# Performance work log

Measured on AMD Instinct MI355X. Metric: run time of the kernel, lower is better.

The kernel has to match this reference:

```python
import jax, jax.numpy as jnp
import numpy as np

B, S, H, E, R, K = 8, 2048, 2048, 8, 16, 3
ALPHA = 0.5
LAMBDA_COV = 0.5
BETA_ENT = 0.1
TEMP_LO, TEMP_HI = 0.5, 1.5
SCALE_T = 2.0   # lora scaling (alpha/r) teacher
SCALE_S = 2.0   # lora scaling student
EPS = 1e-8


def setup_inputs() -> dict:
    key = jax.random.key(0)
    ks = jax.random.split(key, 16)
    tg = jax.random.uniform(ks[0], (B, S, E)) + 1e-3
    tg = tg / tg.sum(-1, keepdims=True)            # teacher gate probabilities
    sg = jax.random.uniform(ks[1], (B, S, E)) + 1e-3
    sg = sg / sg.sum(-1, keepdims=True)            # student gate probabilities
    th = jax.random.normal(ks[2], (B, S, H), jnp.float32)
    sh = jax.random.normal(ks[3], (B, S, H), jnp.float32)
    mask = jnp.ones((B, S), jnp.int32)
    un = jax.random.uniform(ks[4], (K, B, S, E))   # MC sampling noise
    inv = 1.0 / np.sqrt(H)
    W_t = jax.random.normal(ks[5], (H, H), jnp.float32) * inv
    b_t = jnp.zeros((H,), jnp.float32)
    A_t = jax.random.normal(ks[6], (R, H), jnp.float32) * 0.02
    B_t = jax.random.normal(ks[7], (E, H, R), jnp.float32) * 0.02
    W_s = jax.random.normal(ks[8], (H, H), jnp.float32) * inv
    b_s = jnp.zeros((H,), jnp.float32)
    A_s = jax.random.normal(ks[9], (R, H), jnp.float32) * 0.02
    B_s = jax.random.normal(ks[10], (E, H, R), jnp.float32) * 0.02
    temperature = jnp.float32(1.0)
    return dict(teacher_gates=tg, student_gates=sg,
                teacher_hidden_states=th, student_hidden_states=sh,
                attention_mask=mask, uniform_noise=un,
                W_t=W_t, b_t=b_t, A_t=A_t, B_t=B_t,
                W_s=W_s, b_s=b_s, A_s=A_s, B_s=B_s,
                temperature=temperature)


def _mse_all_experts(th, sh, W_t, b_t, A_t, B_t, W_s, b_s, A_s, B_s):
    """MSE(student_expert_hidden, teacher_expert_hidden) for ALL experts at once.
    expert_hidden = x@W^T + b + scale * (x@A^T) @ B_e^T. Expanding the squared
    difference avoids materializing [B,S,E,H]."""
    base_t = th @ W_t.T + b_t                      # [B,S,H]
    base_s = sh @ W_s.T + b_s                      # [B,S,H]
    a_t = th @ A_t.T                               # [B,S,R]
    a_s = sh @ A_s.T                               # [B,S,R]
    d = base_s - base_t                            # [B,S,H]
    mean_base = jnp.mean(d * d, axis=-1)           # [B,S]
    # cross terms: (1/H) d . (scale * a @ B_e^T)
    proj_s = jnp.einsum('bsh,ehr->bser', d, B_s)   # [B,S,E,R]
    proj_t = jnp.einsum('bsh,ehr->bser', d, B_t)
    cross = SCALE_S * jnp.einsum('bser,bsr->bse', proj_s, a_s) \
          - SCALE_T * jnp.einsum('bser,bsr->bse', proj_t, a_t)
    # quadratic lora terms via per-expert Gram matrices [E,R,R]
    G_ss = jnp.einsum('ehr,ehq->erq', B_s, B_s)
    G_st = jnp.einsum('ehr,ehq->erq', B_s, B_t)
    G_tt = jnp.einsum('ehr,ehq->erq', B_t, B_t)
    q_ss = jnp.einsum('bsr,erq,bsq->bse', a_s, G_ss, a_s)
    q_st = jnp.einsum('bsr,erq,bsq->bse', a_s, G_st, a_t)
    q_tt = jnp.einsum('bsr,erq,bsq->bse', a_t, G_tt, a_t)
    quad = SCALE_S * SCALE_S * q_ss - 2.0 * SCALE_S * SCALE_T * q_st + SCALE_T * SCALE_T * q_tt
    return mean_base[..., None] + (2.0 / H) * cross + (1.0 / H) * quad  # [B,S,E]


def _method_a(teacher_gates, student_gates, mse_all, uniform_noise, mask_f):
    """Vectorized MC expert sampling with alpha-renormalization (lax.scan over K)."""
    gumbel = -jnp.log(-jnp.log(uniform_noise * (1.0 - 2e-7) + 1e-7))  # [K,B,S,E]

    def step(p, g):  # p: current (renormalized) probs [B,S,E]
        idx = jnp.argmax(jnp.log(p) + g, axis=-1)          # multinomial sample [B,S]
        oh = jax.nn.one_hot(idx, E, dtype=p.dtype)          # [B,S,E]
        w = jnp.sum(p * oh, -1)                             # importance weight [B,S]
        mse_k = jnp.sum(mse_all * oh, -1)                   # gathered expert MSE
        sg_k = jnp.sum(student_gates * oh, -1)              # student gate at sampled expert
        mw = mask_f * w
        feat = jnp.sum(mw * mse_k)
        wsum = jnp.sum(mw)
        t_counts = jnp.sum(mw[..., None] * oh, axis=(0, 1))           # [E]
        s_counts = jnp.sum((mask_f * sg_k)[..., None] * oh, axis=(0, 1))
        p_new = p * (1.0 + (ALPHA - 1.0) * oh)
        p_new = p_new / jnp.sum(p_new, -1, keepdims=True)
        return p_new, (feat, wsum, t_counts, s_counts)

    _, (feats, wsums, tcs, scs) = jax.lax.scan(step, teacher_gates, gumbel)
    total_feat = feats.sum()
    total_w = wsums.sum()
    t_counts = tcs.sum(0)
    s_counts = scs.sum(0)

    feat_loss = total_feat / jnp.maximum(total_w, 1e-8)
    t_avg = t_counts / t_counts.sum() + EPS
    s_avg = s_counts / s_counts.sum() + EPS
    t_avg = t_avg / t_avg.sum()
    s_avg = s_avg / s_avg.sum()
    # F.kl_div(s.log(), t, reduction='batchmean') on 1-D input divides by E
    coverage_kl = jnp.sum(t_avg * (jnp.log(t_avg) - jnp.log(s_avg))) / E
    return feat_loss, coverage_kl


def reference(teacher_gates, student_gates, teacher_hidden_states, student_hidden_states,
              attention_mask, uniform_noise, W_t, b_t, A_t, B_t, W_s, b_s, A_s, B_s,
              temperature):
    mask_f = attention_mask.astype(teacher_gates.dtype)
    mse_all = _mse_all_experts(teacher_hidden_states, student_hidden_states,
                               W_t, b_t, A_t, B_t, W_s, b_s, A_s, B_s)
    feat_loss, coverage_kl = _method_a(teacher_gates, student_gates, mse_all,
                                       uniform_noise, mask_f)
    method_a_total = feat_loss + LAMBDA_COV * coverage_kl
    # Method B: temperature-entropy router distillation
    temp_c = jnp.clip(temperature, TEMP_LO, TEMP_HI)
    s_temp = jax.nn.softmax(student_gates / temp_c, axis=-1)
    # F.kl_div(s_temp.log(), teacher, 'batchmean') divides by batch dim B
    temp_kl = jnp.sum(teacher_gates * (jnp.log(teacher_gates) - jnp.log(s_temp))) / B
    entropy = -jnp.sum(student_gates * jnp.log(student_gates), axis=-1)
    entropy_loss = -jnp.mean(entropy)
    method_b_total = temp_kl + BETA_ENT * entropy_loss
    # [feat, coverage_kl, method_a_total, temp_kl, entropy, method_b_total, temperature]
    return jnp.stack([feat_loss, coverage_kl, method_a_total,
                      temp_kl, entropy_loss, method_b_total, temp_c])
```

## Files before the change

### kernel.cpp

```cpp
#include <hip/hip_runtime.h>
#include <math.h>

typedef unsigned short u16;
typedef unsigned int u32;
typedef float f32x4 __attribute__((ext_vector_type(4)));
typedef __bf16 bf16x8 __attribute__((ext_vector_type(8)));

#define NTOK 16384
#define HD   2048
#define KX   4096

__device__ __forceinline__ u16 f2bf(float f) {
  u32 u = __float_as_uint(f);
  u32 r = (u + 0x7fffu + ((u >> 16) & 1u)) >> 16;
  return (u16)r;
}
__device__ __forceinline__ float bf2f(u16 s) { return __uint_as_float(((u32)s) << 16); }

__device__ __forceinline__ void gload_lds16(const void* g, void* l) {
  __builtin_amdgcn_global_load_lds((const __attribute__((address_space(1))) u32*)g,
                                   (__attribute__((address_space(3))) u32*)l, 16, 0, 0);
}

__global__ void zero_k(float* a, int n) {
  int i = blockIdx.x * 256 + threadIdx.x;
  if (i < n) a[i] = 0.f;
}

__global__ void make_bias_k(const float* __restrict__ b_t, const float* __restrict__ b_s,
                            float* __restrict__ db) {
  int i = blockIdx.x * 256 + threadIdx.x;
  if (i < HD) db[i] = b_s[i] - b_t[i];
}

__global__ __launch_bounds__(256) void convert_X_k(const float* __restrict__ th,
                                                   const float* __restrict__ sh,
                                                   u16* __restrict__ X) {
  size_t t = (size_t)blockIdx.x * 256 + threadIdx.x;
  int n = (int)(t >> 9);
  int k = ((int)t & 511) * 8;
  const float* src = (k < HD) ? (th + (size_t)n * HD + k) : (sh + (size_t)n * HD + (k - HD));
  float4 v0 = *(const float4*)src;
  float4 v1 = *(const float4*)(src + 4);
  uint4 pk;
  pk.x = (u32)f2bf(v0.x) | ((u32)f2bf(v0.y) << 16);
  pk.y = (u32)f2bf(v0.z) | ((u32)f2bf(v0.w) << 16);
  pk.z = (u32)f2bf(v1.x) | ((u32)f2bf(v1.y) << 16);
  pk.w = (u32)f2bf(v1.z) | ((u32)f2bf(v1.w) << 16);
  *(uint4*)(X + t * 8) = pk;
}

__global__ __launch_bounds__(256) void convert_W_k(const float* __restrict__ W_t,
                                                   const float* __restrict__ W_s,
                                                   const float* __restrict__ A_t,
                                                   const float* __restrict__ A_s,
                                                   u16* __restrict__ Wc,
                                                   u16* __restrict__ WcA) {
  size_t t = (size_t)blockIdx.x * 256 + threadIdx.x;
  int nr = (int)(t >> 9);
  int k = ((int)t & 511) * 8;
  float f[8];
#pragma unroll
  for (int j = 0; j < 8; ++j) f[j] = 0.f;
  u16* dst;
  if (nr < HD) {
    dst = Wc + (size_t)nr * KX + k;
    if (k < HD) {
      const float* s = W_t + (size_t)nr * HD + k;
#pragma unroll
      for (int j = 0; j < 8; ++j) f[j] = -s[j];
    } else {
      const float* s = W_s + (size_t)nr * HD + (k - HD);
#pragma unroll
      for (int j = 0; j < 8; ++j) f[j] = s[j];
    }
  } else {
    int nr2 = nr - HD;
    dst = WcA + (size_t)nr2 * KX + k;
    if (nr2 < 16) {
      if (k < HD) {
        const float* s = A_t + (size_t)nr2 * HD + k;
#pragma unroll
        for (int j = 0; j < 8; ++j) f[j] = s[j];
      }
    } else if (nr2 < 32) {
      if (k >= HD) {
        const float* s = A_s + (size_t)(nr2 - 16) * HD + (k - HD);
#pragma unroll
        for (int j = 0; j < 8; ++j) f[j] = s[j];
      }
    }
  }
  uint4 pk;
  pk.x = (u32)f2bf(f[0]) | ((u32)f2bf(f[1]) << 16);
  pk.y = (u32)f2bf(f[2]) | ((u32)f2bf(f[3]) << 16);
  pk.z = (u32)f2bf(f[4]) | ((u32)f2bf(f[5]) << 16);
  pk.w = (u32)f2bf(f[6]) | ((u32)f2bf(f[7]) << 16);
  *(uint4*)dst = pk;
}

__global__ __launch_bounds__(256) void convert_Bc_k(const float* __restrict__ Bs_,
                                                    const float* __restrict__ Bt_,
                                                    u16* __restrict__ Bc) {
  size_t t = (size_t)blockIdx.x * 256 + threadIdx.x;
  int c = (int)(t >> 8);
  int h = ((int)t & 255) * 8;
  const float* src = (c < 128) ? Bs_ : Bt_;
  int e = (c & 127) >> 4, r = c & 15;
  const float* base = src + (size_t)e * HD * 16 + (size_t)h * 16 + r;
  float f[8];
#pragma unroll
  for (int j = 0; j < 8; ++j) f[j] = base[(size_t)j * 16];
  uint4 pk;
  pk.x = (u32)f2bf(f[0]) | ((u32)f2bf(f[1]) << 16);
  pk.y = (u32)f2bf(f[2]) | ((u32)f2bf(f[3]) << 16);
  pk.z = (u32)f2bf(f[4]) | ((u32)f2bf(f[5]) << 16);
  pk.w = (u32)f2bf(f[6]) | ((u32)f2bf(f[7]) << 16);
  *(uint4*)(Bc + t * 8) = pk;
}

__global__ __launch_bounds__(256) void gram_k(const float* __restrict__ Bs_,
                                              const float* __restrict__ Bt_,
                                              float* __restrict__ grams) {
  __shared__ float ss[128 * 16];
  __shared__ float st[128 * 16];
  const int e = blockIdx.x >> 4;
  const int ch = blockIdx.x & 15;
  const int tid = threadIdx.x;
  const float* bs = Bs_ + (size_t)e * HD * 16 + (size_t)ch * 128 * 16;
  const float* bt = Bt_ + (size_t)e * HD * 16 + (size_t)ch * 128 * 16;
#pragma unroll
  for (int j = 0; j < 8; ++j) {
    int i = tid + j * 256;
    ss[i] = bs[i];
    st[i] = bt[i];
  }
  __syncthreads();
  const int r = tid >> 4, q = tid & 15;
  float gss = 0.f, gst = 0.f, gtt = 0.f;
  for (int hh = 0; hh < 128; ++hh) {
    float vsr = ss[hh * 16 + r], vsq = ss[hh * 16 + q];
    float vtr = st[hh * 16 + r], vtq = st[hh * 16 + q];
    gss += vsr * vsq;
    gst += vsr * vtq;
    gtt += vtr * vtq;
  }
  atomicAdd(&grams[e * 256 + r * 16 + q], gss);
  atomicAdd(&grams[2048 + e * 256 + r * 16 + q], gst);
  atomicAdd(&grams[4096 + e * 256 + r * 16 + q], gtt);
}

__global__ __launch_bounds__(512, 2) void gemm256_k(const u16* __restrict__ A,
                                                    const u16* __restrict__ Bm,
                                                    u16* __restrict__ D,
                                                    const float* __restrict__ bias) {
  __shared__ u16 As[2][16384];
  __shared__ u16 Bs[2][16384];
  const int tid = threadIdx.x;
  const int w = tid >> 6, l = tid & 63;
  const int id = blockIdx.x;
  const int tile = (id & 7) * 64 + (id >> 3);
  const int m0 = (tile & 63) * 256;
  const int n0 = (tile >> 6) * 256;
  const int wm = (w >> 2) * 128;
  const int wn = (w & 3) * 64;

  f32x4 acc[8][4] = {};

  const int rlo = w * 8 + (l >> 3);
  const int csw = ((l & 7) ^ (l >> 3)) * 8;
  const u16* gA = A + (size_t)(m0 + rlo) * KX + csw;
  const u16* gB = Bm + (size_t)(n0 + rlo) * KX + csw;

  for (int t = 0; t < 64; ++t) {
    const int b = t & 1;
    if (t == 0) {
#pragma unroll
      for (int i = 0; i < 4; ++i) {
        gload_lds16(gA + (size_t)i * 64 * KX, &As[0][i * 4096 + w * 512]);
        gload_lds16(gB + (size_t)i * 64 * KX, &Bs[0][i * 4096 + w * 512]);
      }
    }
    __syncthreads();
    if (t < 63) {
      const u16* ga = gA + (size_t)(t + 1) * 64;
      const u16* gb = gB + (size_t)(t + 1) * 64;
#pragma unroll
      for (int i = 0; i < 4; ++i) {
        gload_lds16(ga + (size_t)i * 64 * KX, &As[b ^ 1][i * 4096 + w * 512]);
        gload_lds16(gb + (size_t)i * 64 * KX, &Bs[b ^ 1][i * 4096 + w * 512]);
      }
    }
#pragma unroll
    for (int ks = 0; ks < 2; ++ks) {
      bf16x8 bfr[4], afr[4];
#pragma unroll
      for (int n = 0; n < 4; ++n) {
        int row = wn + n * 16 + (l & 15);
        int off = (row * 64 + ks * 32 + (l >> 4) * 8) ^ ((row & 7) * 8);
        bfr[n] = *(const bf16x8*)&Bs[b][off];
      }
#pragma unroll
      for (int mm = 0; mm < 4; ++mm) {
        int row = wm + mm * 16 + (l & 15);
        int off = (row * 64 + ks * 32 + (l >> 4) * 8) ^ ((row & 7) * 8);
        afr[mm] = *(const bf16x8*)&As[b][off];
      }
      __builtin_amdgcn_s_setprio(1);
#pragma unroll
      for (int mm = 0; mm < 4; ++mm)
#pragma unroll
        for (int n = 0; n < 4; ++n)
          acc[mm][n] = __builtin_amdgcn_mfma_f32_16x16x32_bf16(afr[mm], bfr[n], acc[mm][n], 0, 0, 0);
      __builtin_amdgcn_s_setprio(0);
#pragma unroll
      for (int mm = 0; mm < 4; ++mm) {
        int row = wm + 64 + mm * 16 + (l & 15);
        int off = (row * 64 + ks * 32 + (l >> 4) * 8) ^ ((row & 7) * 8);
        afr[mm] = *(const bf16x8*)&As[b][off];
      }
      __builtin_amdgcn_s_setprio(1);
#pragma unroll
      for (int mm = 0; mm < 4; ++mm)
#pragma unroll
        for (int n = 0; n < 4; ++n)
          acc[4 + mm][n] = __builtin_amdgcn_mfma_f32_16x16x32_bf16(afr[mm], bfr[n], acc[4 + mm][n], 0, 0, 0);
      __builtin_amdgcn_s_setprio(0);
    }
  }

#pragma unroll
  for (int mi = 0; mi < 8; ++mi) {
#pragma unroll
    for (int ni = 0; ni < 4; ++ni) {
      int row0 = m0 + wm + mi * 16 + (l >> 4) * 4;
      int col = n0 + wn + ni * 16 + (l & 15);
      float badd = bias[col];
      f32x4 v = acc[mi][ni];
#pragma unroll
      for (int j = 0; j < 4; ++j)
        D[(size_t)(row0 + j) * HD + col] = f2bf(v[j] + badd);
    }
  }
}

__global__ __launch_bounds__(256) void gemm_bt_k(const u16* __restrict__ A, int lda,
                                                 const u16* __restrict__ Bm, int ldb,
                                                 int K, float* __restrict__ Cp, int ldc,
                                                 int store_n) {
  __shared__ u16 Asl[128 * 32];
  __shared__ u16 Bsl[128 * 32];
  const int tid = threadIdx.x;
  const int wave = tid >> 6;
  const int lane = tid & 63;
  const int m0 = blockIdx.x * 128;
  const int n0 = blockIdx.y * 128;
  const int wm = (wave >> 1) * 64;
  const int wn = (wave & 1) * 64;
  f32x4 acc[4][4] = {};

  const int srow = wave * 32 + (lane >> 2);
  const int scol = (lane & 3) * 8;
  const u16* gA = A + (size_t)(m0 + srow) * lda + scol;
  const u16* gB = Bm + (size_t)(n0 + srow) * ldb + scol;
  u16* lA = Asl + wave * 1024;
  u16* lB = Bsl + wave * 1024;

  for (int k0 = 0; k0 < K; k0 += 32) {
    gload_lds16(gA + k0, lA);
    gload_lds16(gA + k0 + (size_t)16 * lda, lA + 512);
    gload_lds16(gB + k0, lB);
    gload_lds16(gB + k0 + (size_t)16 * ldb, lB + 512);
    __syncthreads();
    bf16x8 af[4], bff[4];
#pragma unroll
    for (int mi = 0; mi < 4; ++mi)
      af[mi] = *(const bf16x8*)&Asl[(wm + mi * 16 + (lane & 15)) * 32 + (lane >> 4) * 8];
#pragma unroll
    for (int ni = 0; ni < 4; ++ni)
      bff[ni] = *(const bf16x8*)&Bsl[(wn + ni * 16 + (lane & 15)) * 32 + (lane >> 4) * 8];
#pragma unroll
    for (int mi = 0; mi < 4; ++mi)
#pragma unroll
      for (int ni = 0; ni < 4; ++ni)
        acc[mi][ni] = __builtin_amdgcn_mfma_f32_16x16x32_bf16(af[mi], bff[ni], acc[mi][ni], 0, 0, 0);
    __syncthreads();
  }

#pragma unroll
  for (int mi = 0; mi < 4; ++mi) {
#pragma unroll
    for (int ni = 0; ni < 4; ++ni) {
      int row0 = m0 + wm + mi * 16 + (lane >> 4) * 4;
      int col = n0 + wn + ni * 16 + (lane & 15);
      if (col < store_n) {
        f32x4 v = acc[mi][ni];
#pragma unroll
        for (int j = 0; j < 4; ++j)
          Cp[(size_t)(row0 + j) * ldc + col] = v[j];
      }
    }
  }
}

__global__ __launch_bounds__(256) void token_k(const u16* __restrict__ D,
                                               const float* __restrict__ aV,
                                               const float* __restrict__ proj,
                                               const float* __restrict__ grams,
                                               const float* __restrict__ tg,
                                               const float* __restrict__ sg,
                                               const float* __restrict__ un,
                                               const int* __restrict__ maskp,
                                               const float* __restrict__ temp,
                                               float* __restrict__ accum) {
  __shared__ float blk[20];
  if (threadIdx.x < 20) blk[threadIdx.x] = 0.f;
  __syncthreads();
  const int wave = threadIdx.x >> 6, lane = threadIdx.x & 63;
  const int n = blockIdx.x * 4 + wave;
  const u16* drow = D + (size_t)n * HD;

  float ssum = 0.f;
#pragma unroll
  for (int j = 0; j < 4; ++j) {
    uint4 v = *(const uint4*)(drow + j * 512 + lane * 8);
    u32 wv;
    float f;
    wv = v.x; f = bf2f((u16)(wv & 0xffff)); ssum += f * f; f = bf2f((u16)(wv >> 16)); ssum += f * f;
    wv = v.y; f = bf2f((u16)(wv & 0xffff)); ssum += f * f; f = bf2f((u16)(wv >> 16)); ssum += f * f;
    wv = v.z; f = bf2f((u16)(wv & 0xffff)); ssum += f * f; f = bf2f((u16)(wv >> 16)); ssum += f * f;
    wv = v.w; f = bf2f((u16)(wv & 0xffff)); ssum += f * f; f = bf2f((u16)(wv >> 16)); ssum += f * f;
  }
#pragma unroll
  for (int m = 1; m < 64; m <<= 1) ssum += __shfl_xor(ssum, m);
  const float mean_base = ssum * (1.0f / (float)HD);

  const float* arow = aV + (size_t)n * 32;
  float a_tv[16], a_sv[16];
#pragma unroll
  for (int r = 0; r < 16; ++r) {
    a_tv[r] = arow[r];
    a_sv[r] = arow[16 + r];
  }

  const int e = lane & 7;
  const int pp = lane >> 3;
  const float* Ps = proj + (size_t)n * 256 + e * 16;
  const float* Pt = Ps + 128;
  const float* Gss = grams + e * 256;
  const float* Gst = grams + 2048 + e * 256;
  const float* Gtt = grams + 4096 + e * 256;
  float crossp = 0.f, qss = 0.f, qst = 0.f, qtt = 0.f;
#pragma unroll
  for (int rr = 0; rr < 2; ++rr) {
    int r = pp * 2 + rr;
    float asr = arow[16 + r];
    float atr = arow[r];
    crossp += 2.0f * Ps[r] * asr - 2.0f * Pt[r] * atr;
    const float* gssr = Gss + r * 16;
    const float* gstr = Gst + r * 16;
    const float* gttr = Gtt + r * 16;
    float vss = 0.f, vst = 0.f, vtt = 0.f;
#pragma unroll
    for (int q = 0; q < 16; ++q) {
      vss += gssr[q] * a_sv[q];
      vst += gstr[q] * a_tv[q];
      vtt += gttr[q] * a_tv[q];
    }
    qss += asr * vss;
    qst += asr * vst;
    qtt += atr * vtt;
  }
#pragma unroll
  for (int m = 8; m < 64; m <<= 1) {
    crossp += __shfl_xor(crossp, m);
    qss += __shfl_xor(qss, m);
    qst += __shfl_xor(qst, m);
    qtt += __shfl_xor(qtt, m);
  }
  float quad = 4.0f * qss - 8.0f * qst + 4.0f * qtt;
  float my_mse = mean_base + (2.0f / (float)HD) * crossp + (1.0f / (float)HD) * quad;

  float p[8], gt[8], gs[8];
#pragma unroll
  for (int i = 0; i < 8; ++i) {
    gt[i] = tg[(size_t)n * 8 + i];
    gs[i] = sg[(size_t)n * 8 + i];
    p[i] = gt[i];
  }
  const float mf = (float)maskp[n];
  float feat = 0.f, wsum = 0.f;
  float tc[8] = {0, 0, 0, 0, 0, 0, 0, 0};
  float sc[8] = {0, 0, 0, 0, 0, 0, 0, 0};
#pragma unroll
  for (int k = 0; k < 3; ++k) {
    int idx = 0;
    float best = -1e30f;
#pragma unroll
    for (int i = 0; i < 8; ++i) {
      float u = un[((size_t)k * NTOK + n) * 8 + i];
      float g = -logf(-logf(u * (1.0f - 2e-7f) + 1e-7f));
      float s = logf(p[i]) + g;
      if (s > best) { best = s; idx = i; }
    }
    float wgt = 0.f, sgi = 0.f;
#pragma unroll
    for (int i = 0; i < 8; ++i)
      if (i == idx) { wgt = p[i]; sgi = gs[i]; }
    float mse_k = __shfl(my_mse, idx);
    feat += mf * wgt * mse_k;
    wsum += mf * wgt;
#pragma unroll
    for (int i = 0; i < 8; ++i)
      if (i == idx) { tc[i] += mf * wgt; sc[i] += mf * sgi; }
    float sum = 0.f;
#pragma unroll
    for (int i = 0; i < 8; ++i) {
      if (i == idx) p[i] *= 0.5f;
      sum += p[i];
    }
#pragma unroll
    for (int i = 0; i < 8; ++i) p[i] /= sum;
  }

  float tcl = fminf(fmaxf(temp[0], 0.5f), 1.5f);
  float invt = 1.0f / tcl;
  float x[8];
  float xm = -1e30f;
#pragma unroll
  for (int i = 0; i < 8; ++i) { x[i] = gs[i] * invt; xm = fmaxf(xm, x[i]); }
  float sx = 0.f;
#pragma unroll
  for (int i = 0; i < 8; ++i) sx += expf(x[i] - xm);
  float lse = xm + logf(sx);
  float tkl = 0.f, ent = 0.f;
#pragma unroll
  for (int i = 0; i < 8; ++i) {
    tkl += gt[i] * (logf(gt[i]) - (x[i] - lse));
    ent -= gs[i] * logf(gs[i]);
  }

  if (lane == 0) {
    atomicAdd(&blk[0], feat);
    atomicAdd(&blk[1], wsum);
#pragma unroll
    for (int i = 0; i < 8; ++i) {
      atomicAdd(&blk[2 + i], tc[i]);
      atomicAdd(&blk[10 + i], sc[i]);
    }
    atomicAdd(&blk[18], tkl);
    atomicAdd(&blk[19], ent);
  }
  __syncthreads();
  if (threadIdx.x < 20) atomicAdd(&accum[threadIdx.x], blk[threadIdx.x]);
}

__global__ void finalize_k(const float* __restrict__ accum, const float* __restrict__ temp,
                           float* __restrict__ out) {
  if (threadIdx.x != 0 || blockIdx.x != 0) return;
  float feat = accum[0] / fmaxf(accum[1], 1e-8f);
  float tsum = 0.f, ssum = 0.f;
  for (int e2 = 0; e2 < 8; ++e2) { tsum += accum[2 + e2]; ssum += accum[10 + e2]; }
  float ta[8], sa[8];
  float tas = 0.f, sas = 0.f;
  for (int e2 = 0; e2 < 8; ++e2) {
    ta[e2] = accum[2 + e2] / tsum + 1e-8f; tas += ta[e2];
    sa[e2] = accum[10 + e2] / ssum + 1e-8f; sas += sa[e2];
  }
  float cov = 0.f;
  for (int e2 = 0; e2 < 8; ++e2) {
    float tt = ta[e2] / tas, sv = sa[e2] / sas;
    cov += tt * (logf(tt) - logf(sv));
  }
  cov /= 8.0f;
  float tcl = fminf(fmaxf(temp[0], 0.5f), 1.5f);
  float tkl = accum[18] / 8.0f;
  float entl = -accum[19] / (float)NTOK;
  out[0] = feat;
  out[1] = cov;
  out[2] = feat + 0.5f * cov;
  out[3] = tkl;
  out[4] = entl;
  out[5] = tkl + 0.1f * entl;
  out[6] = tcl;
}

extern "C" void kernel_launch(void* const* d_in, const int* in_sizes, int n_in,
                              void* d_out, int out_size, void* d_ws, size_t ws_size,
                              hipStream_t stream) {
  const float* tg = (const float*)d_in[0];
  const float* sg = (const float*)d_in[1];
  const float* th = (const float*)d_in[2];
  const float* sh = (const float*)d_in[3];
  const int* mask = (const int*)d_in[4];
  const float* un = (const float*)d_in[5];
  const float* W_t = (const float*)d_in[6];
  const float* b_t = (const float*)d_in[7];
  const float* A_t = (const float*)d_in[8];
  const float* B_t = (const float*)d_in[9];
  const float* W_s = (const float*)d_in[10];
  const float* b_s = (const float*)d_in[11];
  const float* A_s = (const float*)d_in[12];
  const float* B_s = (const float*)d_in[13];
  const float* temp = (const float*)d_in[14];
  float* out = (float*)d_out;

  char* ws = (char*)d_ws;
  const size_t OFF_X = 0;
  const size_t OFF_W = OFF_X + (size_t)NTOK * KX * 2;
  const size_t OFF_WA = OFF_W + (size_t)HD * KX * 2;
  const size_t OFF_D = OFF_WA + (size_t)128 * KX * 2;
  const size_t OFF_BC = OFF_D + (size_t)NTOK * HD * 2;
  const size_t OFF_PJ = OFF_BC + (size_t)256 * HD * 2;
  const size_t OFF_AV = OFF_PJ + (size_t)NTOK * 256 * 4;
  const size_t OFF_GR = OFF_AV + (size_t)NTOK * 32 * 4;
  const size_t OFF_AC = OFF_GR + 6144 * 4;
  const size_t OFF_BI = OFF_AC + 128;

  u16* X = (u16*)(ws + OFF_X);
  u16* Wc = (u16*)(ws + OFF_W);
  u16* WcA = (u16*)(ws + OFF_WA);
  u16* D = (u16*)(ws + OFF_D);
  u16* Bc = (u16*)(ws + OFF_BC);
  float* proj = (float*)(ws + OFF_PJ);
  float* aV = (float*)(ws + OFF_AV);
  float* grams = (float*)(ws + OFF_GR);
  float* accum = (float*)(ws + OFF_AC);
  float* dbias = (float*)(ws + OFF_BI);

  zero_k<<<25, 256, 0, stream>>>(grams, 6176);
  make_bias_k<<<8, 256, 0, stream>>>(b_t, b_s, dbias);
  convert_X_k<<<32768, 256, 0, stream>>>(th, sh, X);
  convert_W_k<<<4352, 256, 0, stream>>>(W_t, W_s, A_t, A_s, Wc, WcA);
  convert_Bc_k<<<256, 256, 0, stream>>>(B_s, B_t, Bc);
  gram_k<<<128, 256, 0, stream>>>(B_s, B_t, grams);

  gemm256_k<<<512, 512, 0, stream>>>(X, Wc, D, dbias);
  gemm_bt_k<<<dim3(128, 1), 256, 0, stream>>>(X, KX, WcA, KX, KX, aV, 32, 32);
  gemm_bt_k<<<dim3(128, 2), 256, 0, stream>>>(D, HD, Bc, HD, HD, proj, 256, 256);

  token_k<<<4096, 256, 0, stream>>>(D, aV, proj, grams, tg, sg, un, mask, temp, accum);
  finalize_k<<<1, 64, 0, stream>>>(accum, temp, out);
}
```

Baseline: 864.9 us.

## Merge prep kernels into one launch and fold LoRA-A GEMM into main GEMM

Six conversion and setup kernels are combined into a single prep kernel that dispatches on block index. The gram computation now runs one block per expert over the full hidden dimension and writes results directly, with no atomics or zeroing pass. The main 256x256 GEMM switches from a 2-stage, 64-wide K pipeline to a 4-stage, 32-wide K pipeline with explicit vmcnt waits and a new LDS swizzle. Its grid grows by 128 blocks that compute the small X·A^T projection in place of the separate gemm_bt launch. This cuts launch count and may overlap the small GEMM with the large one, but the extra blocks use a simple unpipelined loop and the new pipeline has more barriers per K.

```diff
diff --git a/kernel.cpp b/kernel.cpp
--- a/kernel.cpp
+++ b/kernel.cpp
@@ -22,224 +22,263 @@
                                    (__attribute__((address_space(3))) u32*)l, 16, 0, 0);
 }
 
-__global__ void zero_k(float* a, int n) {
-  int i = blockIdx.x * 256 + threadIdx.x;
-  if (i < n) a[i] = 0.f;
-}
-
-__global__ void make_bias_k(const float* __restrict__ b_t, const float* __restrict__ b_s,
-                            float* __restrict__ db) {
-  int i = blockIdx.x * 256 + threadIdx.x;
-  if (i < HD) db[i] = b_s[i] - b_t[i];
-}
-
-__global__ __launch_bounds__(256) void convert_X_k(const float* __restrict__ th,
-                                                   const float* __restrict__ sh,
-                                                   u16* __restrict__ X) {
-  size_t t = (size_t)blockIdx.x * 256 + threadIdx.x;
-  int n = (int)(t >> 9);
-  int k = ((int)t & 511) * 8;
-  const float* src = (k < HD) ? (th + (size_t)n * HD + k) : (sh + (size_t)n * HD + (k - HD));
-  float4 v0 = *(const float4*)src;
-  float4 v1 = *(const float4*)(src + 4);
-  uint4 pk;
-  pk.x = (u32)f2bf(v0.x) | ((u32)f2bf(v0.y) << 16);
-  pk.y = (u32)f2bf(v0.z) | ((u32)f2bf(v0.w) << 16);
-  pk.z = (u32)f2bf(v1.x) | ((u32)f2bf(v1.y) << 16);
-  pk.w = (u32)f2bf(v1.z) | ((u32)f2bf(v1.w) << 16);
-  *(uint4*)(X + t * 8) = pk;
-}
-
-__global__ __launch_bounds__(256) void convert_W_k(const float* __restrict__ W_t,
-                                                   const float* __restrict__ W_s,
-                                                   const float* __restrict__ A_t,
-                                                   const float* __restrict__ A_s,
-                                                   u16* __restrict__ Wc,
-                                                   u16* __restrict__ WcA) {
-  size_t t = (size_t)blockIdx.x * 256 + threadIdx.x;
-  int nr = (int)(t >> 9);
-  int k = ((int)t & 511) * 8;
-  float f[8];
-#pragma unroll
-  for (int j = 0; j < 8; ++j) f[j] = 0.f;
-  u16* dst;
-  if (nr < HD) {
-    dst = Wc + (size_t)nr * KX + k;
-    if (k < HD) {
-      const float* s = W_t + (size_t)nr * HD + k;
-#pragma unroll
-      for (int j = 0; j < 8; ++j) f[j] = -s[j];
-    } else {
-      const float* s = W_s + (size_t)nr * HD + (k - HD);
-#pragma unroll
-      for (int j = 0; j < 8; ++j) f[j] = s[j];
-    }
+__global__ __launch_bounds__(256) void prep_k(const float* __restrict__ th,
+                                              const float* __restrict__ sh,
+                                              const float* __restrict__ W_t,
+                                              const float* __restrict__ W_s,
+                                              const float* __restrict__ A_t,
+                                              const float* __restrict__ A_s,
+                                              const float* __restrict__ Bs_,
+                                              const float* __restrict__ Bt_,
+                                              const float* __restrict__ b_t,
+                                              const float* __restrict__ b_s,
+                                              u16* __restrict__ X,
+                                              u16* __restrict__ Wc,
+                                              u16* __restrict__ WcA,
+                                              u16* __restrict__ Bc,
+                                              float* __restrict__ grams,
+                                              float* __restrict__ accum,
+                                              float* __restrict__ dbias) {
+  __shared__ float sbuf[4096];
+  const int id = blockIdx.x;
+  const int tid = threadIdx.x;
+
+  if (id < 2048) {
+    for (size_t t = (size_t)id * 256 + tid; t < (size_t)8388608; t += (size_t)2048 * 256) {
+      int n = (int)(t >> 9);
+      int k = ((int)t & 511) * 8;
+      const float* src = (k < HD) ? (th + (size_t)n * HD + k) : (sh + (size_t)n * HD + (k - HD));
+      float4 v0 = *(const float4*)src;
+      float4 v1 = *(const float4*)(src + 4);
+      uint4 pk;
+      pk.x = (u32)f2bf(v0.x) | ((u32)f2bf(v0.y) << 16);
+      pk.y = (u32)f2bf(v0.z) | ((u32)f2bf(v0.w) << 16);
+      pk.z = (u32)f2bf(v1.x) | ((u32)f2bf(v1.y) << 16);
+      pk.w = (u32)f2bf(v1.z) | ((u32)f2bf(v1.w) << 16);
+      *(uint4*)(X + t * 8) = pk;
+    }
+  } else if (id < 3136) {
+    int b = id - 2048;
+#pragma unroll
+    for (int it = 0; it < 4; ++it) {
+      size_t t = (size_t)(b * 4 + it) * 256 + tid;
+      int nr = (int)(t >> 9);
+      int k = ((int)t & 511) * 8;
+      float f[8];
+#pragma unroll
+      for (int j = 0; j < 8; ++j) f[j] = 0.f;
+      u16* dst;
+      if (nr < HD) {
+        dst = Wc + (size_t)nr * KX + k;
+        if (k < HD) {
+          const float* s = W_t + (size_t)nr * HD + k;
+#pragma unroll
+          for (int j = 0; j < 8; ++j) f[j] = -s[j];
+        } else {
+          const float* s = W_s + (size_t)nr * HD + (k - HD);
+#pragma unroll
+          for (int j = 0; j < 8; ++j) f[j] = s[j];
+        }
+      } else {
+        int nr2 = nr - HD;
+        dst = WcA + (size_t)nr2 * KX + k;
+        if (nr2 < 16) {
+          if (k < HD) {
+            const float* s = A_t + (size_t)nr2 * HD + k;
+#pragma unroll
+            for (int j = 0; j < 8; ++j) f[j] = s[j];
+          }
+        } else if (nr2 < 32) {
+          if (k >= HD) {
+            const float* s = A_s + (size_t)(nr2 - 16) * HD + (k - HD);
+#pragma unroll
+            for (int j = 0; j < 8; ++j) f[j] = s[j];
+          }
+        }
+      }
+      uint4 pk;
+      pk.x = (u32)f2bf(f[0]) | ((u32)f2bf(f[1]) << 16);
+      pk.y = (u32)f2bf(f[2]) | ((u32)f2bf(f[3]) << 16);
+      pk.z = (u32)f2bf(f[4]) | ((u32)f2bf(f[5]) << 16);
+      pk.w = (u32)f2bf(f[6]) | ((u32)f2bf(f[7]) << 16);
+      *(uint4*)dst = pk;
+    }
+  } else if (id < 3392) {
+    size_t t = (size_t)(id - 3136) * 256 + tid;
+    int c = (int)(t >> 8);
+    int h = ((int)t & 255) * 8;
+    const float* src = (c < 128) ? Bs_ : Bt_;
+    int e = (c & 127) >> 4, r = c & 15;
+    const float* base = src + (size_t)e * HD * 16 + (size_t)h * 16 + r;
+    float f[8];
+#pragma unroll
+    for (int j = 0; j < 8; ++j) f[j] = base[(size_t)j * 16];
+    uint4 pk;
+    pk.x = (u32)f2bf(f[0]) | ((u32)f2bf(f[1]) << 16);
+    pk.y = (u32)f2bf(f[2]) | ((u32)f2bf(f[3]) << 16);
+    pk.z = (u32)f2bf(f[4]) | ((u32)f2bf(f[5]) << 16);
+    pk.w = (u32)f2bf(f[6]) | ((u32)f2bf(f[7]) << 16);
+    *(uint4*)(Bc + t * 8) = pk;
+  } else if (id < 3400) {
+    const int e = id - 3392;
+    float* ss = sbuf;
+    float* st = sbuf + 2048;
+    const float* bs = Bs_ + (size_t)e * HD * 16;
+    const float* bt = Bt_ + (size_t)e * HD * 16;
+    const int r = tid >> 4, q = tid & 15;
+    float gss = 0.f, gst = 0.f, gtt = 0.f;
+    for (int h0 = 0; h0 < HD; h0 += 128) {
+      __syncthreads();
+#pragma unroll
+      for (int j = 0; j < 8; ++j) {
+        int i = tid + j * 256;
+        ss[i] = bs[(size_t)h0 * 16 + i];
+        st[i] = bt[(size_t)h0 * 16 + i];
+      }
+      __syncthreads();
+      for (int hh = 0; hh < 128; ++hh) {
+        float vsr = ss[hh * 16 + r], vsq = ss[hh * 16 + q];
+        float vtr = st[hh * 16 + r], vtq = st[hh * 16 + q];
+        gss += vsr * vsq;
+        gst += vsr * vtq;
+        gtt += vtr * vtq;
+      }
+    }
+    grams[e * 256 + r * 16 + q] = gss;
+    grams[2048 + e * 256 + r * 16 + q] = gst;
+    grams[4096 + e * 256 + r * 16 + q] = gtt;
   } else {
-    int nr2 = nr - HD;
-    dst = WcA + (size_t)nr2 * KX + k;
-    if (nr2 < 16) {
-      if (k < HD) {
-        const float* s = A_t + (size_t)nr2 * HD + k;
-#pragma unroll
-        for (int j = 0; j < 8; ++j) f[j] = s[j];
-      }
-    } else if (nr2 < 32) {
-      if (k >= HD) {
-        const float* s = A_s + (size_t)(nr2 - 16) * HD + (k - HD);
-#pragma unroll
-        for (int j = 0; j < 8; ++j) f[j] = s[j];
-      }
-    }
-  }
-  uint4 pk;
-  pk.x = (u32)f2bf(f[0]) | ((u32)f2bf(f[1]) << 16);
-  pk.y = (u32)f2bf(f[2]) | ((u32)f2bf(f[3]) << 16);
-  pk.z = (u32)f2bf(f[4]) | ((u32)f2bf(f[5]) << 16);
-  pk.w = (u32)f2bf(f[6]) | ((u32)f2bf(f[7]) << 16);
-  *(uint4*)dst = pk;
-}
-
-__global__ __launch_bounds__(256) void convert_Bc_k(const float* __restrict__ Bs_,
-                                                    const float* __restrict__ Bt_,
-                                                    u16* __restrict__ Bc) {
-  size_t t = (size_t)blockIdx.x * 256 + threadIdx.x;
-  int c = (int)(t >> 8);
-  int h = ((int)t & 255) * 8;
-  const float* src = (c < 128) ? Bs_ : Bt_;
-  int e = (c & 127) >> 4, r = c & 15;
-  const float* base = src + (size_t)e * HD * 16 + (size_t)h * 16 + r;
-  float f[8];
-#pragma unroll
-  for (int j = 0; j < 8; ++j) f[j] = base[(size_t)j * 16];
-  uint4 pk;
-  pk.x = (u32)f2bf(f[0]) | ((u32)f2bf(f[1]) << 16);
-  pk.y = (u32)f2bf(f[2]) | ((u32)f2bf(f[3]) << 16);
-  pk.z = (u32)f2bf(f[4]) | ((u32)f2bf(f[5]) << 16);
-  pk.w = (u32)f2bf(f[6]) | ((u32)f2bf(f[7]) << 16);
-  *(uint4*)(Bc + t * 8) = pk;
-}
-
-__global__ __launch_bounds__(256) void gram_k(const float* __restrict__ Bs_,
-                                              const float* __restrict__ Bt_,
-                                              float* __restrict__ grams) {
-  __shared__ float ss[128 * 16];
-  __shared__ float st[128 * 16];
-  const int e = blockIdx.x >> 4;
-  const int ch = blockIdx.x & 15;
-  const int tid = threadIdx.x;
-  const float* bs = Bs_ + (size_t)e * HD * 16 + (size_t)ch * 128 * 16;
-  const float* bt = Bt_ + (size_t)e * HD * 16 + (size_t)ch * 128 * 16;
-#pragma unroll
-  for (int j = 0; j < 8; ++j) {
-    int i = tid + j * 256;
-    ss[i] = bs[i];
-    st[i] = bt[i];
-  }
-  __syncthreads();
-  const int r = tid >> 4, q = tid & 15;
-  float gss = 0.f, gst = 0.f, gtt = 0.f;
-  for (int hh = 0; hh < 128; ++hh) {
-    float vsr = ss[hh * 16 + r], vsq = ss[hh * 16 + q];
-    float vtr = st[hh * 16 + r], vtq = st[hh * 16 + q];
-    gss += vsr * vsq;
-    gst += vsr * vtq;
-    gtt += vtr * vtq;
-  }
-  atomicAdd(&grams[e * 256 + r * 16 + q], gss);
-  atomicAdd(&grams[2048 + e * 256 + r * 16 + q], gst);
-  atomicAdd(&grams[4096 + e * 256 + r * 16 + q], gtt);
+    int i = (id - 3400) * 256 + tid;
+    if (i < 2048) dbias[i] = b_s[i] - b_t[i];
+    else if (i < 2080) accum[i - 2048] = 0.f;
+  }
 }
 
 __global__ __launch_bounds__(512, 2) void gemm256_k(const u16* __restrict__ A,
                                                     const u16* __restrict__ Bm,
+                                                    const u16* __restrict__ WcA,
                                                     u16* __restrict__ D,
+                                                    float* __restrict__ aV,
                                                     const float* __restrict__ bias) {
-  __shared__ u16 As[2][16384];
-  __shared__ u16 Bs[2][16384];
+  __shared__ u16 As[4][8192];
+  __shared__ u16 Bs[4][8192];
   const int tid = threadIdx.x;
   const int w = tid >> 6, l = tid & 63;
+  const int lr = l & 15, lc = l >> 4;
   const int id = blockIdx.x;
-  const int tile = (id & 7) * 64 + (id >> 3);
-  const int m0 = (tile & 63) * 256;
-  const int n0 = (tile >> 6) * 256;
-  const int wm = (w >> 2) * 128;
-  const int wn = (w & 3) * 64;
-
-  f32x4 acc[8][4] = {};
-
-  const int rlo = w * 8 + (l >> 3);
-  const int csw = ((l & 7) ^ (l >> 3)) * 8;
-  const u16* gA = A + (size_t)(m0 + rlo) * KX + csw;
-  const u16* gB = Bm + (size_t)(n0 + rlo) * KX + csw;
-
-  for (int t = 0; t < 64; ++t) {
-    const int b = t & 1;
-    if (t == 0) {
-#pragma unroll
-      for (int i = 0; i < 4; ++i) {
-        gload_lds16(gA + (size_t)i * 64 * KX, &As[0][i * 4096 + w * 512]);
-        gload_lds16(gB + (size_t)i * 64 * KX, &Bs[0][i * 4096 + w * 512]);
-      }
-    }
-    __syncthreads();
-    if (t < 63) {
-      const u16* ga = gA + (size_t)(t + 1) * 64;
-      const u16* gb = gB + (size_t)(t + 1) * 64;
-#pragma unroll
-      for (int i = 0; i < 4; ++i) {
-        gload_lds16(ga + (size_t)i * 64 * KX, &As[b ^ 1][i * 4096 + w * 512]);
-        gload_lds16(gb + (size_t)i * 64 * KX, &Bs[b ^ 1][i * 4096 + w * 512]);
-      }
-    }
-#pragma unroll
-    for (int ks = 0; ks < 2; ++ks) {
-      bf16x8 bfr[4], afr[4];
-#pragma unroll
-      for (int n = 0; n < 4; ++n) {
-        int row = wn + n * 16 + (l & 15);
-        int off = (row * 64 + ks * 32 + (l >> 4) * 8) ^ ((row & 7) * 8);
-        bfr[n] = *(const bf16x8*)&Bs[b][off];
-      }
-#pragma unroll
-      for (int mm = 0; mm < 4; ++mm) {
-        int row = wm + mm * 16 + (l & 15);
-        int off = (row * 64 + ks * 32 + (l >> 4) * 8) ^ ((row & 7) * 8);
-        afr[mm] = *(const bf16x8*)&As[b][off];
+
+  const int srow = w * 16 + (l >> 2);
+  const int gslot = (l & 3) ^ ((l >> 3) & 3);
+
+  if (id < 512) {
+    const int tile = (id & 7) * 64 + (id >> 3);
+    const int m0 = (tile & 63) * 256;
+    const int n0 = (tile >> 6) * 256;
+    const int wm = (w >> 2) * 128;
+    const int wn = (w & 3) * 64;
+
+    f32x4 acc[8][4] = {};
+
+    const u16* gA = A + (size_t)(m0 + srow) * KX + gslot * 8;
+    const u16* gB = Bm + (size_t)(n0 + srow) * KX + gslot * 8;
+
+#define STAGE(s)                                                        \
+  {                                                                     \
+    const int buf_ = (s) & 3;                                           \
+    const size_t ko_ = (size_t)(s) * 32;                                \
+    gload_lds16(gA + ko_, &As[buf_][w * 512]);                          \
+    gload_lds16(gA + ko_ + (size_t)128 * KX, &As[buf_][4096 + w * 512]);\
+    gload_lds16(gB + ko_, &Bs[buf_][w * 512]);                          \
+    gload_lds16(gB + ko_ + (size_t)128 * KX, &Bs[buf_][4096 + w * 512]);\
+  }
+
+    STAGE(0);
+    STAGE(1);
+
+    for (int s = 0; s < 128; ++s) {
+      if (s + 2 < 128) STAGE(s + 2);
+      if (s < 126)       asm volatile("s_waitcnt vmcnt(8)\n\ts_barrier" ::: "memory");
+      else if (s == 126) asm volatile("s_waitcnt vmcnt(4)\n\ts_barrier" ::: "memory");
+      else               asm volatile("s_waitcnt vmcnt(0)\n\ts_barrier" ::: "memory");
+      const int buf = s & 3;
+      bf16x8 af[8], bfr[4];
+#pragma unroll
+      for (int ni = 0; ni < 4; ++ni) {
+        int R = wn + ni * 16 + lr;
+        bfr[ni] = *(const bf16x8*)&Bs[buf][R * 32 + ((lc ^ ((R >> 1) & 3)) * 8)];
+      }
+#pragma unroll
+      for (int mi = 0; mi < 8; ++mi) {
+        int R = wm + mi * 16 + lr;
+        af[mi] = *(const bf16x8*)&As[buf][R * 32 + ((lc ^ ((R >> 1) & 3)) * 8)];
       }
       __builtin_amdgcn_s_setprio(1);
 #pragma unroll
-      for (int mm = 0; mm < 4; ++mm)
-#pragma unroll
-        for (int n = 0; n < 4; ++n)
-          acc[mm][n] = __builtin_amdgcn_mfma_f32_16x16x32_bf16(afr[mm], bfr[n], acc[mm][n], 0, 0, 0);
+      for (int mi = 0; mi < 8; ++mi)
+#pragma unroll
+        for (int ni = 0; ni < 4; ++ni)
+          acc[mi][ni] = __builtin_amdgcn_mfma_f32_16x16x32_bf16(af[mi], bfr[ni], acc[mi][ni], 0, 0, 0);
       __builtin_amdgcn_s_setprio(0);
-#pragma unroll
-      for (int mm = 0; mm < 4; ++mm) {
-        int row = wm + 64 + mm * 16 + (l & 15);
-        int off = (row * 64 + ks * 32 + (l >> 4) * 8) ^ ((row & 7) * 8);
-        afr[mm] = *(const bf16x8*)&As[b][off];
-      }
-      __builtin_amdgcn_s_setprio(1);
-#pragma unroll
-      for (int mm = 0; mm < 4; ++mm)
-#pragma unroll
-        for (int n = 0; n < 4; ++n)
-          acc[4 + mm][n] = __builtin_amdgcn_mfma_f32_16x16x32_bf16(afr[mm], bfr[n], acc[4 + mm][n], 0, 0, 0);
-      __builtin_amdgcn_s_setprio(0);
-    }
-  }
-
-#pragma unroll
-  for (int mi = 0; mi < 8; ++mi) {
-#pragma unroll
-    for (int ni = 0; ni < 4; ++ni) {
-      int row0 = m0 + wm + mi * 16 + (l >> 4) * 4;
-      int col = n0 + wn + ni * 16 + (l & 15);
-      float badd = bias[col];
-      f32x4 v = acc[mi][ni];
-#pragma unroll
-      for (int j = 0; j < 4; ++j)
-        D[(size_t)(row0 + j) * HD + col] = f2bf(v[j] + badd);
+    }
+#undef STAGE
+
+#pragma unroll
+    for (int mi = 0; mi < 8; ++mi) {
+#pragma unroll
+      for (int ni = 0; ni < 4; ++ni) {
+        int row0 = m0 + wm + mi * 16 + lc * 4;
+        int col = n0 + wn + ni * 16 + lr;
+        float badd = bias[col];
+        f32x4 v = acc[mi][ni];
+#pragma unroll
+        for (int j = 0; j < 4; ++j)
+          D[(size_t)(row0 + j) * HD + col] = f2bf(v[j] + badd);
+      }
+    }
+  } else {
+    const int m0a = (id - 512) * 128;
+    const int wm2 = (w >> 2) * 64;
+    const int wn2 = (w & 3) * 32;
+    f32x4 acc2[4][2] = {};
+    const u16* gA2 = A + (size_t)(m0a + srow) * KX + gslot * 8;
+    const u16* gB2 = WcA + (size_t)srow * KX + gslot * 8;
+
+    for (int k0 = 0; k0 < KX; k0 += 32) {
+      gload_lds16(gA2 + k0, &As[0][w * 512]);
+      gload_lds16(gB2 + k0, &Bs[0][w * 512]);
+      __syncthreads();
+      bf16x8 af2[4], bf2[2];
+#pragma unroll
+      for (int mi = 0; mi < 4; ++mi) {
+        int R = wm2 + mi * 16 + lr;
+        af2[mi] = *(const bf16x8*)&As[0][R * 32 + ((lc ^ ((R >> 1) & 3)) * 8)];
+      }
+#pragma unroll
+      for (int ni = 0; ni < 2; ++ni) {
+        int R = wn2 + ni * 16 + lr;
+        bf2[ni] = *(const bf16x8*)&Bs[0][R * 32 + ((lc ^ ((R >> 1) & 3)) * 8)];
+      }
+#pragma unroll
+      for (int mi = 0; mi < 4; ++mi)
+#pragma unroll
+        for (int ni = 0; ni < 2; ++ni)
+          acc2[mi][ni] = __builtin_amdgcn_mfma_f32_16x16x32_bf16(af2[mi], bf2[ni], acc2[mi][ni], 0, 0, 0);
+      __syncthreads();
+    }
+
+    if ((w & 3) == 0) {
+#pragma unroll
+      for (int mi = 0; mi < 4; ++mi) {
+#pragma unroll
+        for (int ni = 0; ni < 2; ++ni) {
+          int row0 = m0a + wm2 + mi * 16 + lc * 4;
+          int col = ni * 16 + lr;
+          f32x4 v = acc2[mi][ni];
+#pragma unroll
+          for (int j = 0; j < 4; ++j)
+            aV[(size_t)(row0 + j) * 32 + col] = v[j];
+        }
+      }
     }
   }
 }
@@ -528,15 +567,9 @@
   float* accum = (float*)(ws + OFF_AC);
   float* dbias = (float*)(ws + OFF_BI);
 
-  zero_k<<<25, 256, 0, stream>>>(grams, 6176);
-  make_bias_k<<<8, 256, 0, stream>>>(b_t, b_s, dbias);
-  convert_X_k<<<32768, 256, 0, stream>>>(th, sh, X);
-  convert_W_k<<<4352, 256, 0, stream>>>(W_t, W_s, A_t, A_s, Wc, WcA);
-  convert_Bc_k<<<256, 256, 0, stream>>>(B_s, B_t, Bc);
-  gram_k<<<128, 256, 0, stream>>>(B_s, B_t, grams);
-
-  gemm256_k<<<512, 512, 0, stream>>>(X, Wc, D, dbias);
-  gemm_bt_k<<<dim3(128, 1), 256, 0, stream>>>(X, KX, WcA, KX, KX, aV, 32, 32);
+  prep_k<<<3409, 256, 0, stream>>>(th, sh, W_t, W_s, A_t, A_s, B_s, B_t, b_t, b_s,
+                                   X, Wc, WcA, Bc, grams, accum, dbias);
+  gemm256_k<<<640, 512, 0, stream>>>(X, Wc, WcA, D, aV, dbias);
   gemm_bt_k<<<dim3(128, 2), 256, 0, stream>>>(D, HD, Bc, HD, HD, proj, 256, 256);
 
   token_k<<<4096, 256, 0, stream>>>(D, aV, proj, grams, tg, sg, un, mask, temp, accum);
```

Result: no change. 870.0 us (+0.6%).
